# Kernel tuning notes

Hardware: AMD Instinct MI355X
Metric: run time of the kernel (lower is better)

## Reference

```python
import jax, jax.numpy as jnp
import numpy as np

B, LAGS, POOL, D, H, NTS = 16, 4096, 4, 512, 8, 1000
S = LAGS // POOL          # num_pools = 1024
DH = D // H               # head dim = 64


def _layernorm_dim1(x, gamma, beta, eps=1e-5):
    # torch code: mean/var over dim=1 (channel axis), unbiased var, per-position affine
    mean = jnp.mean(x, axis=1, keepdims=True)
    var = jnp.var(x, axis=1, keepdims=True, ddof=1)
    unit = (x - mean) / jnp.sqrt(eps + var)
    return gamma * unit + beta


def setup_inputs() -> dict:
    key = jax.random.key(0)
    ks = jax.random.split(key, 16)
    inp = {
        "ts": jax.random.normal(ks[0], (B, 1, LAGS), dtype=jnp.float32),
        "te": jax.random.randint(ks[1], (B, 1), 0, NTS),
        "conv_w": jax.random.normal(ks[2], (D, 1, POOL), dtype=jnp.float32) * (1.0 / POOL) ** 0.5,
        "conv_b": jax.random.normal(ks[3], (D,), dtype=jnp.float32) * 0.02,
        "pe_emb": jax.random.normal(ks[4], (S, D), dtype=jnp.float32),
        "ts_emb": jax.random.normal(ks[5], (NTS, D), dtype=jnp.float32),
        "ln1_g": jnp.ones((S,), dtype=jnp.float32),
        "ln1_b": jnp.zeros((S,), dtype=jnp.float32),
        "dense_M": jax.random.normal(ks[6], (D, D), dtype=jnp.float32) * D ** -0.5,
        "Wq": jax.random.normal(ks[7], (H, DH, D), dtype=jnp.float32) * D ** -0.5,
        "Wk": jax.random.normal(ks[8], (H, DH, D), dtype=jnp.float32) * D ** -0.5,
        "Wv": jax.random.normal(ks[9], (H, DH, D), dtype=jnp.float32) * D ** -0.5,
        "Wo": jax.random.normal(ks[10], (D, D), dtype=jnp.float32) * D ** -0.5,
        "bo": jnp.zeros((D, 1), dtype=jnp.float32),
        "ln2_g": jnp.ones((S,), dtype=jnp.float32),
        "ln2_b": jnp.zeros((S,), dtype=jnp.float32),
    }
    return inp


def _forward(ts, te, conv_w, conv_b, pe_emb, ts_emb, ln1_g, ln1_b,
             dense_M, Wq, Wk, Wv, Wo, bo, ln2_g, ln2_b):
    # Conv1d with stride == kernel_size: non-overlapping patches
    xr = ts.reshape(B, S, POOL)                                   # (B,S,P)
    conv = jnp.einsum('bsp,dp->bds', xr, conv_w[:, 0, :]) + conv_b[:, None]  # (B,D,S)
    conv = conv + pe_emb.T                                        # positional add (D,S)
    act = jax.nn.gelu(conv, approximate=False)
    n1 = _layernorm_dim1(act, ln1_g, ln1_b)
    dense = jnp.einsum('ed,bds->bes', dense_M, n1)                # Linear: M @ x
    dense = dense + ts_emb[te[:, 0]][:, :, None]                  # ts embedding (B,D,1)

    # multi-head attention, Q=K=V=dense; vectorized over heads
    Qd = jnp.einsum('hcd,bds->bhcs', Wq, dense)                   # (B,H,DH,S)
    Kd = jnp.einsum('hcd,bds->bhcs', Wk, dense)
    Vd = jnp.einsum('hcd,bds->bhcs', Wv, dense)
    scores = jnp.einsum('bhci,bhcj->bhij', Qd, Kd) / DH ** 0.5    # (B,H,S,S)
    i_idx = jnp.arange(S)
    mask = i_idx[:, None] > i_idx[None, :]                        # tril(diagonal=-1): i>j -> -inf
    scores = jnp.where(mask, -jnp.inf, scores)
    sm = jax.nn.softmax(scores, axis=2)                           # softmax over dim 1 of (S,S)
    attn = jnp.einsum('bhci,bhij->bhcj', Vd, sm)                  # V @ softmaxed
    cat = attn.reshape(B, D, S)                                   # concat heads on dim 1
    out = jnp.einsum('ed,bds->bes', Wo, cat) + bo[None]           # final linear + bias
    res = out + conv                                              # residual
    return _layernorm_dim1(res, ln2_g, ln2_b)


def reference(ts, te, conv_w, conv_b, pe_emb, ts_emb, ln1_g, ln1_b,
              dense_M, Wq, Wk, Wv, Wo, bo, ln2_g, ln2_b):
    return _forward(ts, te, conv_w, conv_b, pe_emb, ts_emb, ln1_g, ln1_b,
                    dense_M, Wq, Wk, Wv, Wo, bo, ln2_g, ln2_b)
```

## Files before the change

kernel.cpp:

```cpp
#include <hip/hip_runtime.h>
#include <hip/hip_bf16.h>

#define B_ 16
#define S_ 1024
#define D_ 512
#define H_ 8
#define DH_ 64

typedef __attribute__((ext_vector_type(8))) short bf16x8;
typedef __attribute__((ext_vector_type(4))) short bf16x4;
typedef __attribute__((ext_vector_type(4))) float f32x4;
typedef __attribute__((ext_vector_type(16))) float f32x16;

__device__ __forceinline__ short f2bf(float f) {
    __hip_bfloat16 h = __float2bfloat16(f);
    return *reinterpret_cast<short*>(&h);
}
__device__ __forceinline__ float bf2f(short s) {
    unsigned u = ((unsigned)(unsigned short)s) << 16;
    return __uint_as_float(u);
}
__device__ __forceinline__ unsigned pack_bf2(float lo, float hi) {
    unsigned a = (unsigned)(unsigned short)f2bf(lo);
    unsigned b = (unsigned)(unsigned short)f2bf(hi);
    return a | (b << 16);
}
__device__ __forceinline__ void gload16(const void* g, void* l) {
    __builtin_amdgcn_global_load_lds(
        (const __attribute__((address_space(1))) unsigned int*)g,
        (__attribute__((address_space(3))) unsigned int*)l, 16, 0, 0);
}

__global__ __launch_bounds__(256) void prep_w(
    const float* __restrict__ M, const float* __restrict__ Wq,
    const float* __restrict__ Wk, const float* __restrict__ Wv,
    const float* __restrict__ Wo, __hip_bfloat16* __restrict__ wb)
{
    __hip_bfloat16* wsrc = wb;
    __hip_bfloat16* Wob  = wb + 786432;
    __hip_bfloat16* MT   = wb + 1048576;

    const int blk = blockIdx.x, t = threadIdx.x;
    if (blk < 512) {
        const int wi = blk >> 7;
        const int off = (blk & 127) * 2048 + t * 8;
        const float* src = (wi == 0) ? Wq : (wi == 1) ? Wk : (wi == 2) ? Wv : Wo;
        const float scale = (wi == 0) ? 0.18033688011112042f : 1.0f;
        const float4 f0 = *reinterpret_cast<const float4*>(src + off);
        const float4 f1 = *reinterpret_cast<const float4*>(src + off + 4);
        const float fv[8] = {f0.x, f0.y, f0.z, f0.w, f1.x, f1.y, f1.z, f1.w};
        union { short s[8]; bf16x8 v; } r;
#pragma unroll
        for (int j = 0; j < 8; ++j) r.s[j] = f2bf(fv[j] * scale);
        __hip_bfloat16* dst = (wi == 3) ? (Wob + off) : (wsrc + wi * 262144 + off);
        *reinterpret_cast<bf16x8*>(dst) = r.v;
    } else {
        __shared__ float tile[32][33];
        const int tt = blk - 512;
        const int e0 = (tt & 15) * 32, d0 = (tt >> 4) * 32;
        const int r = t >> 5, c = t & 31;
#pragma unroll
        for (int k = 0; k < 4; ++k)
            tile[r + k * 8][c] = M[(size_t)(e0 + r + k * 8) * 512 + d0 + c];
        __syncthreads();
#pragma unroll
        for (int k = 0; k < 4; ++k)
            MT[(size_t)(d0 + r + k * 8) * 512 + e0 + c] =
                __float2bfloat16(tile[c][r + k * 8]);
    }
}

__global__ __launch_bounds__(256) void bias_k(
    const __hip_bfloat16* __restrict__ wsrc, const float* __restrict__ ts_emb,
    const int* __restrict__ te, float* __restrict__ qkvpart)
{
    const int blk = blockIdx.x;
    const int w16b = blk >> 2, dc = blk & 3;
    const int b = w16b & 15, w = w16b >> 4;
    const float* e = ts_emb + (size_t)te[b] * 512 + dc * 128;
#pragma unroll
    for (int rep = 0; rep < 2; ++rep) {
        const int n = threadIdx.x + rep * 256;
        const __hip_bfloat16* wr = wsrc + ((size_t)(w * 512 + n)) * 512 + dc * 128;
        float s = 0.f;
#pragma unroll 4
        for (int d8 = 0; d8 < 128; d8 += 8) {
            const bf16x8 wv8 = *reinterpret_cast<const bf16x8*>(wr + d8);
            const float4 e0 = *reinterpret_cast<const float4*>(e + d8);
            const float4 e1 = *reinterpret_cast<const float4*>(e + d8 + 4);
            s += bf2f(wv8[0]) * e0.x + bf2f(wv8[1]) * e0.y
               + bf2f(wv8[2]) * e0.z + bf2f(wv8[3]) * e0.w
               + bf2f(wv8[4]) * e1.x + bf2f(wv8[5]) * e1.y
               + bf2f(wv8[6]) * e1.z + bf2f(wv8[7]) * e1.w;
        }
        qkvpart[(size_t)dc * 24576 + (size_t)w16b * 512 + n] = s;
    }
}

__global__ __launch_bounds__(256) void k1_conv_gelu_ln(
    const float* __restrict__ ts, const float* __restrict__ conv_w,
    const float* __restrict__ conv_b, const float* __restrict__ pe,
    const float* __restrict__ g1, const float* __restrict__ b1,
    __hip_bfloat16* __restrict__ n1)
{
    const int w = threadIdx.x >> 6, lane = threadIdx.x & 63;
    const int row = blockIdx.x * 4 + w;
    const int b = row >> 10, s = row & 1023;
    const float4 x = *reinterpret_cast<const float4*>(ts + b * 4096 + s * 4);
    const int d0 = lane * 8;

    const float4 cb0 = *reinterpret_cast<const float4*>(conv_b + d0);
    const float4 cb1 = *reinterpret_cast<const float4*>(conv_b + d0 + 4);
    const float4 pe0 = *reinterpret_cast<const float4*>(pe + s * 512 + d0);
    const float4 pe1 = *reinterpret_cast<const float4*>(pe + s * 512 + d0 + 4);
    const float cbv[8] = {cb0.x, cb0.y, cb0.z, cb0.w, cb1.x, cb1.y, cb1.z, cb1.w};
    const float pev[8] = {pe0.x, pe0.y, pe0.z, pe0.w, pe1.x, pe1.y, pe1.z, pe1.w};

    float a[8];
    float sum = 0.f, sq = 0.f;
#pragma unroll
    for (int j = 0; j < 8; ++j) {
        const float4 wv = *reinterpret_cast<const float4*>(conv_w + (d0 + j) * 4);
        float v = x.x * wv.x + x.y * wv.y + x.z * wv.z + x.w * wv.w
                + cbv[j] + pev[j];
        v = 0.5f * v * (1.0f + erff(v * 0.70710678118654752f));
        a[j] = v; sum += v; sq += v * v;
    }
#pragma unroll
    for (int off = 1; off < 64; off <<= 1) {
        sum += __shfl_xor(sum, off);
        sq  += __shfl_xor(sq, off);
    }
    const float mean = sum * (1.0f / 512.0f);
    const float var  = (sq - 512.0f * mean * mean) * (1.0f / 511.0f);
    const float rstd = rsqrtf(var + 1e-5f);
    const float gg = g1[s], bb = b1[s];
    union { short sh[8]; bf16x8 v; } o;
#pragma unroll
    for (int j = 0; j < 8; ++j)
        o.sh[j] = f2bf(gg * ((a[j] - mean) * rstd) + bb);
    *reinterpret_cast<bf16x8*>(n1 + (size_t)row * 512 + d0) = o.v;
}

template<int MODE>
__global__ __launch_bounds__(256, 2) void gemm_k(
    const __hip_bfloat16* __restrict__ A,
    const __hip_bfloat16* __restrict__ Wb,
    void* __restrict__ outp,
    const float* __restrict__ aux)
{
    __shared__ char lA[2][128 * 128];
    __shared__ char lB[2][128 * 128];

    const int t = threadIdx.x;
    const int lane = t & 63;
    const int w = t >> 6;
    const int wm = w & 1, wn = w >> 1;
    const int Rb = blockIdx.x * 128;
    const int Nb = blockIdx.y * 128;
    const int g = lane >> 4, lr = lane & 15;
    const int lrow = lane >> 3;
    const int coff = ((lane & 7) ^ lrow) * 8;

    const __hip_bfloat16* asrc = A  + (size_t)(Rb + lrow) * 512 + coff;
    const __hip_bfloat16* bsrc = Wb + (size_t)(Nb + lrow) * 512 + coff;

    f32x4 acc[4][4];
#pragma unroll
    for (int i = 0; i < 4; ++i)
#pragma unroll
        for (int j = 0; j < 4; ++j) acc[i][j] = {0.f, 0.f, 0.f, 0.f};

    auto stage = [&](int buf, int k0) {
#pragma unroll
        for (int i = 0; i < 4; ++i) {
            const int r0 = w * 32 + i * 8;
            gload16(asrc + (size_t)r0 * 512 + k0, &lA[buf][r0 * 128]);
        }
#pragma unroll
        for (int i = 0; i < 4; ++i) {
            const int r0 = w * 32 + i * 8;
            gload16(bsrc + (size_t)r0 * 512 + k0, &lB[buf][r0 * 128]);
        }
    };

    stage(0, 0);
    __syncthreads();

    for (int kt = 0; kt < 8; ++kt) {
        const int buf = kt & 1;
        if (kt < 7) stage(buf ^ 1, (kt + 1) * 64);
#pragma unroll
        for (int kk = 0; kk < 2; ++kk) {
            bf16x8 af[4], bfv[4];
            const int ch = kk * 4 + g;
#pragma unroll
            for (int mt = 0; mt < 4; ++mt) {
                const int row = wm * 64 + mt * 16 + lr;
                af[mt] = *reinterpret_cast<const bf16x8*>(
                    &lA[buf][row * 128 + ((ch ^ (row & 7)) << 4)]);
            }
#pragma unroll
            for (int nt = 0; nt < 4; ++nt) {
                const int row = wn * 64 + nt * 16 + lr;
                bfv[nt] = *reinterpret_cast<const bf16x8*>(
                    &lB[buf][row * 128 + ((ch ^ (row & 7)) << 4)]);
            }
#pragma unroll
            for (int mt = 0; mt < 4; ++mt)
#pragma unroll
                for (int nt = 0; nt < 4; ++nt)
                    acc[mt][nt] = __builtin_amdgcn_mfma_f32_16x16x32_bf16(
                        af[mt], bfv[nt], acc[mt][nt], 0, 0, 0);
        }
        __syncthreads();
    }

    const int w3 = Nb >> 9;
#pragma unroll
    for (int mt = 0; mt < 4; ++mt) {
#pragma unroll
        for (int nt = 0; nt < 4; ++nt) {
#pragma unroll
            for (int r = 0; r < 4; ++r) {
                const int R = Rb + wm * 64 + mt * 16 + 4 * g + r;
                const int N = Nb + wn * 64 + nt * 16 + lr;
                float v = acc[mt][nt][r];
                if (MODE == 5) {
                    const int Nl = N & 511;
                    const int b = R >> 10, s = R & 1023, h = Nl >> 6, c = Nl & 63;
                    const float* qp = aux + (size_t)(w3 * 16 + b) * 512 + Nl;
                    v += qp[0] + qp[24576] + qp[49152] + qp[73728];
                    __hip_bfloat16* base =
                        reinterpret_cast<__hip_bfloat16*>(outp) + (size_t)w3 * 8388608;
                    if (w3 == 2)
                        base[(((size_t)(b * 8 + h)) * 64 + c) * 1024 + s] =
                            __float2bfloat16(v);
                    else
                        base[(((size_t)(b * 8 + h)) * 1024 + s) * 64 + c] =
                            __float2bfloat16(v);
                } else if (MODE == 6) {
                    reinterpret_cast<__hip_bfloat16*>(outp)[(size_t)R * 512 + N] =
                        __float2bfloat16(v);
                } else {
                    reinterpret_cast<float*>(outp)[(size_t)R * 512 + N] = v + aux[N];
                }
            }
        }
    }
}

__device__ __forceinline__ void write_strip(
    __hip_bfloat16* __restrict__ dstbase, const int jw0,
    const f32x16& o0, const f32x16& o1, const float lsum,
    const int l5, const int ln31)
{
    const float linv = 1.0f / lsum;
#pragma unroll
    for (int r = 0; r < 16; ++r) {
        const int jrow = (r & 3) + 8 * (r >> 2) + 4 * l5;
        const float rinv = __shfl(linv, jrow);
        __hip_bfloat16* dst = dstbase + (size_t)(jw0 + jrow) * 512;
        dst[ln31]      = __float2bfloat16(o0[r] * rinv);
        dst[32 + ln31] = __float2bfloat16(o1[r] * rinv);
    }
}

__global__ __launch_bounds__(256, 4) void attn5_k(
    const __hip_bfloat16* __restrict__ Qm,
    const __hip_bfloat16* __restrict__ Km,
    const __hip_bfloat16* __restrict__ Vt,
    __hip_bfloat16* __restrict__ cat)
{
    __shared__ char qbuf[2][4096];
    __shared__ char vbuf[2][4096];

    const int t = threadIdx.x, lane = t & 63, w = t >> 6;
    const int l5 = lane >> 5, ln31 = lane & 31;
    const int id = blockIdx.x;
    const int bh = id & 127;
    const int jb = (0x32451067u >> ((id >> 7) * 4)) & 7;
    const int b = bh >> 3, h = bh & 7;
    const int j0 = jb * 128 + w * 32;

    const __hip_bfloat16* Qh = Qm + (size_t)bh * (S_ * 64);
    const __hip_bfloat16* Kh = Km + (size_t)bh * (S_ * 64);
    const __hip_bfloat16* Vh = Vt + (size_t)bh * (64 * S_);

    bf16x8 kf[4];
#pragma unroll
    for (int kt = 0; kt < 4; ++kt)
        kf[kt] = *reinterpret_cast<const bf16x8*>(
            Kh + (size_t)(j0 + ln31) * 64 + kt * 16 + l5 * 8);

    f32x16 o0, o1;
#pragma unroll
    for (int r = 0; r < 16; ++r) { o0[r] = 0.f; o1[r] = 0.f; }
    float m = -3e38f, lsum = 0.f;

    const int last = jb * 4 + w;
    const int ntiles = jb * 4 + 4;

    const int q_row  = w * 8 + (lane >> 3);
    const int q_ch   = (lane & 7) ^ (lane >> 3);
    const int v_row  = w * 16 + (lane >> 2);
    const int v_ch   = (lane & 3) ^ ((lane >> 2) & 3) ^ ((lane >> 4) & 3);
    const __hip_bfloat16* qsrc = Qh + (size_t)q_row * 64 + q_ch * 8;
    const __hip_bfloat16* vsrc = Vh + (size_t)v_row * 1024 + v_ch * 8;

    auto stage = [&](int buf, int tile) {
        const int i0 = tile * 32;
        gload16(qsrc + (size_t)i0 * 64, &qbuf[buf][w * 1024]);
        gload16(vsrc + i0,              &vbuf[buf][w * 1024]);
    };

    stage(0, 0);
    __syncthreads();

    for (int tt = 0; tt < ntiles; ++tt) {
        const int buf = tt & 1;
        if (tt + 1 < ntiles) stage(buf ^ 1, tt + 1);
        if (tt <= last) {
            f32x16 sc;
#pragma unroll
            for (int r = 0; r < 16; ++r) sc[r] = 0.f;
            bf16x8 qf[4];
#pragma unroll
            for (int kt = 0; kt < 4; ++kt)
                qf[kt] = *reinterpret_cast<const bf16x8*>(
                    &qbuf[buf][ln31 * 128 + (((kt * 2 + l5) ^ (ln31 & 7)) << 4)]);
#pragma unroll
            for (int kt = 0; kt < 4; ++kt)
                sc = __builtin_amdgcn_mfma_f32_32x32x16_bf16(qf[kt], kf[kt], sc, 0, 0, 0);

            union u8 { bf16x4 h[2]; bf16x8 v; };
            u8 vf[2][2];
#pragma unroll
            for (int kt = 0; kt < 2; ++kt) {
#pragma unroll
                for (int dh = 0; dh < 2; ++dh) {
                    const int drow = ln31 + dh * 32;
                    const int swz = (drow & 3) ^ ((drow >> 2) & 3);
                    const int x0 = kt * 32 + 8 * l5;
#pragma unroll
                    for (int hp = 0; hp < 2; ++hp) {
                        const int x = x0 + hp * 16;
                        vf[kt][dh].h[hp] = *reinterpret_cast<const bf16x4*>(
                            &vbuf[buf][drow * 64 + (((x >> 4) ^ swz) << 4) + (x & 15)]);
                    }
                }
            }

            const bool diag = (tt == last);
            float p[16];
            float mx = -3e38f;
            if (diag) {
#pragma unroll
                for (int r = 0; r < 16; ++r) {
                    const int irow = (r & 3) + 8 * (r >> 2) + 4 * l5;
                    const float v = (irow > ln31) ? -3e38f : sc[r];
                    p[r] = v; mx = fmaxf(mx, v);
                }
            } else {
#pragma unroll
                for (int r = 0; r < 16; ++r) { p[r] = sc[r]; mx = fmaxf(mx, sc[r]); }
            }
            mx = fmaxf(mx, __shfl_xor(mx, 32));
            if (!__all(mx <= m + 8.0f)) {
                const float mn = fmaxf(m, mx);
                const float alpha = exp2f(m - mn);
                m = mn; lsum *= alpha;
#pragma unroll
                for (int r = 0; r < 16; ++r) {
                    const int jrow = (r & 3) + 8 * (r >> 2) + 4 * l5;
                    const float ar = __shfl(alpha, jrow);
                    o0[r] *= ar; o1[r] *= ar;
                }
            }
            float ps = 0.f;
#pragma unroll
            for (int r = 0; r < 16; ++r) { p[r] = exp2f(p[r] - m); ps += p[r]; }
            ps += __shfl_xor(ps, 32);
            lsum += ps;

            union { unsigned u[4]; bf16x8 v; } pa0, pa1;
            pa0.u[0] = pack_bf2(p[0],  p[1]);  pa0.u[1] = pack_bf2(p[2],  p[3]);
            pa0.u[2] = pack_bf2(p[4],  p[5]);  pa0.u[3] = pack_bf2(p[6],  p[7]);
            pa1.u[0] = pack_bf2(p[8],  p[9]);  pa1.u[1] = pack_bf2(p[10], p[11]);
            pa1.u[2] = pack_bf2(p[12], p[13]); pa1.u[3] = pack_bf2(p[14], p[15]);
            o0 = __builtin_amdgcn_mfma_f32_32x32x16_bf16(pa0.v, vf[0][0].v, o0, 0, 0, 0);
            o1 = __builtin_amdgcn_mfma_f32_32x32x16_bf16(pa0.v, vf[0][1].v, o1, 0, 0, 0);
            o0 = __builtin_amdgcn_mfma_f32_32x32x16_bf16(pa1.v, vf[1][0].v, o0, 0, 0, 0);
            o1 = __builtin_amdgcn_mfma_f32_32x32x16_bf16(pa1.v, vf[1][1].v, o1, 0, 0, 0);
        }
        __syncthreads();
    }

    __hip_bfloat16* dstbase = cat + (size_t)b * 1024 * 512 + h * 64;
    write_strip(dstbase, j0, o0, o1, lsum, l5, ln31);
}

__global__ __launch_bounds__(256) void k5_res_ln(
    const float* __restrict__ outf,
    const float* __restrict__ ts, const float* __restrict__ conv_w,
    const float* __restrict__ conv_b, const float* __restrict__ pe,
    const float* __restrict__ g2, const float* __restrict__ b2,
    float* __restrict__ out)
{
    __shared__ float tile[16 * 520];
    const int blk = blockIdx.x;
    const int b = blk >> 6, s0 = (blk & 63) * 16;
    const int t = threadIdx.x;
    const int sl = t >> 4, c = t & 15;
    const int s = s0 + sl;

    const float4 x = *reinterpret_cast<const float4*>(ts + b * 4096 + s * 4);
    float vals[32];
    float sum = 0.f, sq = 0.f;
#pragma unroll
    for (int j = 0; j < 32; ++j) {
        const int d = c + 16 * j;
        const float4 wv = *reinterpret_cast<const float4*>(conv_w + d * 4);
        const float conv = x.x * wv.x + x.y * wv.y + x.z * wv.z + x.w * wv.w
                         + conv_b[d] + pe[s * 512 + d];
        const float a = outf[(size_t)(b * 1024 + s) * 512 + d] + conv;
        vals[j] = a; sum += a; sq += a * a;
    }
#pragma unroll
    for (int off = 1; off < 16; off <<= 1) {
        sum += __shfl_xor(sum, off);
        sq  += __shfl_xor(sq, off);
    }
    const float mean = sum * (1.0f / 512.0f);
    const float var  = (sq - 512.0f * mean * mean) * (1.0f / 511.0f);
    const float rstd = rsqrtf(var + 1e-5f);
    const float gg = g2[s], bb = b2[s];
#pragma unroll
    for (int j = 0; j < 32; ++j) {
        const int d = c + 16 * j;
        tile[sl * 520 + d] = gg * ((vals[j] - mean) * rstd) + bb;
    }
    __syncthreads();
#pragma unroll
    for (int q2 = 0; q2 < 2; ++q2) {
        const int d = t + q2 * 256;
        float buf[16];
#pragma unroll
        for (int sl2 = 0; sl2 < 16; ++sl2) buf[sl2] = tile[sl2 * 520 + d];
        float4* dst = reinterpret_cast<float4*>(
            out + ((size_t)b * 512 + d) * 1024 + s0);
        dst[0] = make_float4(buf[0],  buf[1],  buf[2],  buf[3]);
        dst[1] = make_float4(buf[4],  buf[5],  buf[6],  buf[7]);
        dst[2] = make_float4(buf[8],  buf[9],  buf[10], buf[11]);
        dst[3] = make_float4(buf[12], buf[13], buf[14], buf[15]);
    }
}

extern "C" void kernel_launch(void* const* d_in, const int* in_sizes, int n_in,
                              void* d_out, int out_size, void* d_ws, size_t ws_size,
                              hipStream_t stream)
{
    const float* ts     = (const float*)d_in[0];
    const int*   te     = (const int*)d_in[1];
    const float* conv_w = (const float*)d_in[2];
    const float* conv_b = (const float*)d_in[3];
    const float* pe     = (const float*)d_in[4];
    const float* ts_emb = (const float*)d_in[5];
    const float* g1     = (const float*)d_in[6];
    const float* b1     = (const float*)d_in[7];
    const float* M      = (const float*)d_in[8];
    const float* Wq     = (const float*)d_in[9];
    const float* Wk     = (const float*)d_in[10];
    const float* Wv     = (const float*)d_in[11];
    const float* Wo     = (const float*)d_in[12];
    const float* bo     = (const float*)d_in[13];
    const float* g2     = (const float*)d_in[14];
    const float* b2     = (const float*)d_in[15];

    char* ws = (char*)d_ws;
    __hip_bfloat16* wb     = (__hip_bfloat16*)(ws);
    __hip_bfloat16* wsrc   = wb;
    __hip_bfloat16* Wob    = wb + 786432;
    __hip_bfloat16* MT     = wb + 1048576;
    __hip_bfloat16* Wqkvp  = (__hip_bfloat16*)(ws + (2688ull << 10));
    float*          qkvpart= (float*)(ws + (4608ull << 10));
    __hip_bfloat16* n1     = (__hip_bfloat16*)(ws + ( 6ull << 20));
    __hip_bfloat16* cat    = n1;
    __hip_bfloat16* q      = (__hip_bfloat16*)(ws + (22ull << 20));
    __hip_bfloat16* k      = (__hip_bfloat16*)(ws + (38ull << 20));
    __hip_bfloat16* vT     = (__hip_bfloat16*)(ws + (54ull << 20));
    float*          outf   = (float*)(ws + (22ull << 20));

    prep_w<<<768, 256, 0, stream>>>(M, Wq, Wk, Wv, Wo, wb);
    bias_k<<<192, 256, 0, stream>>>(wsrc, ts_emb, te, qkvpart);
    gemm_k<6><<<dim3(12, 4), 256, 0, stream>>>(wsrc, MT, Wqkvp, nullptr);
    k1_conv_gelu_ln<<<4096, 256, 0, stream>>>(ts, conv_w, conv_b, pe, g1, b1, n1);
    gemm_k<5><<<dim3(128, 12), 256, 0, stream>>>(n1, Wqkvp, q, qkvpart);
    attn5_k<<<1024, 256, 0, stream>>>(q, k, vT, cat);
    gemm_k<3><<<dim3(128, 4), 256, 0, stream>>>(cat, Wob, outf, bo);
    k5_res_ln<<<1024, 256, 0, stream>>>(outf, ts, conv_w, conv_b, pe, g2, b2,
                                        (float*)d_out);
}
```

Measured before the change: 174.3 us.

## Single-buffer GEMM LDS, pair causal attention blocks, store out-proj in bf16

The GEMM kernel drops LDS double buffering in favour of a single buffer with a sync per k-tile, which halves shared memory so the launch bound can rise to 4 blocks per CU. This trades away load/compute overlap for occupancy. The attention kernel now runs 512 blocks, each handling a short and a long causal query block (jb and 7-jb) in sequence, to balance the triangular workload. Separately, the output projection is stored as bf16 rather than fp32 and read back in the residual LayerNorm, which halves that traffic at some precision cost.

Result: slower. 181.4 us (+4.1%).

```diff
diff --git a/kernel.cpp b/kernel.cpp
--- a/kernel.cpp
+++ b/kernel.cpp
@@ -143,14 +143,14 @@
 }
 
 template<int MODE>
-__global__ __launch_bounds__(256, 2) void gemm_k(
+__global__ __launch_bounds__(256, 4) void gemm_k(
     const __hip_bfloat16* __restrict__ A,
     const __hip_bfloat16* __restrict__ Wb,
     void* __restrict__ outp,
     const float* __restrict__ aux)
 {
-    __shared__ char lA[2][128 * 128];
-    __shared__ char lB[2][128 * 128];
+    __shared__ char lA[128 * 128];
+    __shared__ char lB[128 * 128];
 
     const int t = threadIdx.x;
     const int lane = t & 63;
@@ -171,25 +171,19 @@
 #pragma unroll
         for (int j = 0; j < 4; ++j) acc[i][j] = {0.f, 0.f, 0.f, 0.f};
 
-    auto stage = [&](int buf, int k0) {
+    for (int kt = 0; kt < 8; ++kt) {
+        const int k0 = kt * 64;
 #pragma unroll
         for (int i = 0; i < 4; ++i) {
             const int r0 = w * 32 + i * 8;
-            gload16(asrc + (size_t)r0 * 512 + k0, &lA[buf][r0 * 128]);
+            gload16(asrc + (size_t)r0 * 512 + k0, &lA[r0 * 128]);
         }
 #pragma unroll
         for (int i = 0; i < 4; ++i) {
             const int r0 = w * 32 + i * 8;
-            gload16(bsrc + (size_t)r0 * 512 + k0, &lB[buf][r0 * 128]);
+            gload16(bsrc + (size_t)r0 * 512 + k0, &lB[r0 * 128]);
         }
-    };
-
-    stage(0, 0);
-    __syncthreads();
-
-    for (int kt = 0; kt < 8; ++kt) {
-        const int buf = kt & 1;
-        if (kt < 7) stage(buf ^ 1, (kt + 1) * 64);
+        __syncthreads();
 #pragma unroll
         for (int kk = 0; kk < 2; ++kk) {
             bf16x8 af[4], bfv[4];
@@ -198,13 +192,13 @@
             for (int mt = 0; mt < 4; ++mt) {
                 const int row = wm * 64 + mt * 16 + lr;
                 af[mt] = *reinterpret_cast<const bf16x8*>(
-                    &lA[buf][row * 128 + ((ch ^ (row & 7)) << 4)]);
+                    &lA[row * 128 + ((ch ^ (row & 7)) << 4)]);
             }
 #pragma unroll
             for (int nt = 0; nt < 4; ++nt) {
                 const int row = wn * 64 + nt * 16 + lr;
                 bfv[nt] = *reinterpret_cast<const bf16x8*>(
-                    &lB[buf][row * 128 + ((ch ^ (row & 7)) << 4)]);
+                    &lB[row * 128 + ((ch ^ (row & 7)) << 4)]);
             }
 #pragma unroll
             for (int mt = 0; mt < 4; ++mt)
@@ -243,7 +237,8 @@
                     reinterpret_cast<__hip_bfloat16*>(outp)[(size_t)R * 512 + N] =
                         __float2bfloat16(v);
                 } else {
-                    reinterpret_cast<float*>(outp)[(size_t)R * 512 + N] = v + aux[N];
+                    reinterpret_cast<__hip_bfloat16*>(outp)[(size_t)R * 512 + N] =
+                        __float2bfloat16(v + aux[N]);
                 }
             }
         }
@@ -266,7 +261,7 @@
     }
 }
 
-__global__ __launch_bounds__(256, 4) void attn5_k(
+__global__ __launch_bounds__(256, 2) void attn6_k(
     const __hip_bfloat16* __restrict__ Qm,
     const __hip_bfloat16* __restrict__ Km,
     const __hip_bfloat16* __restrict__ Vt,
@@ -279,27 +274,12 @@
     const int l5 = lane >> 5, ln31 = lane & 31;
     const int id = blockIdx.x;
     const int bh = id & 127;
-    const int jb = (0x32451067u >> ((id >> 7) * 4)) & 7;
+    const int sidx = id >> 7;
     const int b = bh >> 3, h = bh & 7;
-    const int j0 = jb * 128 + w * 32;
 
     const __hip_bfloat16* Qh = Qm + (size_t)bh * (S_ * 64);
     const __hip_bfloat16* Kh = Km + (size_t)bh * (S_ * 64);
     const __hip_bfloat16* Vh = Vt + (size_t)bh * (64 * S_);
-
-    bf16x8 kf[4];
-#pragma unroll
-    for (int kt = 0; kt < 4; ++kt)
-        kf[kt] = *reinterpret_cast<const bf16x8*>(
-            Kh + (size_t)(j0 + ln31) * 64 + kt * 16 + l5 * 8);
-
-    f32x16 o0, o1;
-#pragma unroll
-    for (int r = 0; r < 16; ++r) { o0[r] = 0.f; o1[r] = 0.f; }
-    float m = -3e38f, lsum = 0.f;
-
-    const int last = jb * 4 + w;
-    const int ntiles = jb * 4 + 4;
 
     const int q_row  = w * 8 + (lane >> 3);
     const int q_ch   = (lane & 7) ^ (lane >> 3);
@@ -307,6 +287,7 @@
     const int v_ch   = (lane & 3) ^ ((lane >> 2) & 3) ^ ((lane >> 4) & 3);
     const __hip_bfloat16* qsrc = Qh + (size_t)q_row * 64 + q_ch * 8;
     const __hip_bfloat16* vsrc = Vh + (size_t)v_row * 1024 + v_ch * 8;
+    __hip_bfloat16* dstbase = cat + (size_t)b * 1024 * 512 + h * 64;
 
     auto stage = [&](int buf, int tile) {
         const int i0 = tile * 32;
@@ -314,94 +295,112 @@
         gload16(vsrc + i0,              &vbuf[buf][w * 1024]);
     };
 
-    stage(0, 0);
-    __syncthreads();
-
-    for (int tt = 0; tt < ntiles; ++tt) {
-        const int buf = tt & 1;
-        if (tt + 1 < ntiles) stage(buf ^ 1, tt + 1);
-        if (tt <= last) {
-            f32x16 sc;
-#pragma unroll
-            for (int r = 0; r < 16; ++r) sc[r] = 0.f;
-            bf16x8 qf[4];
-#pragma unroll
-            for (int kt = 0; kt < 4; ++kt)
-                qf[kt] = *reinterpret_cast<const bf16x8*>(
-                    &qbuf[buf][ln31 * 128 + (((kt * 2 + l5) ^ (ln31 & 7)) << 4)]);
-#pragma unroll
-            for (int kt = 0; kt < 4; ++kt)
-                sc = __builtin_amdgcn_mfma_f32_32x32x16_bf16(qf[kt], kf[kt], sc, 0, 0, 0);
-
-            union u8 { bf16x4 h[2]; bf16x8 v; };
-            u8 vf[2][2];
-#pragma unroll
-            for (int kt = 0; kt < 2; ++kt) {
-#pragma unroll
-                for (int dh = 0; dh < 2; ++dh) {
-                    const int drow = ln31 + dh * 32;
-                    const int swz = (drow & 3) ^ ((drow >> 2) & 3);
-                    const int x0 = kt * 32 + 8 * l5;
-#pragma unroll
-                    for (int hp = 0; hp < 2; ++hp) {
-                        const int x = x0 + hp * 16;
-                        vf[kt][dh].h[hp] = *reinterpret_cast<const bf16x4*>(
-                            &vbuf[buf][drow * 64 + (((x >> 4) ^ swz) << 4) + (x & 15)]);
+    for (int ph = 0; ph < 2; ++ph) {
+        const int jb = ph ? (7 - sidx) : sidx;
+        const int j0 = jb * 128 + w * 32;
+
+        bf16x8 kf[4];
+#pragma unroll
+        for (int kt = 0; kt < 4; ++kt)
+            kf[kt] = *reinterpret_cast<const bf16x8*>(
+                Kh + (size_t)(j0 + ln31) * 64 + kt * 16 + l5 * 8);
+
+        f32x16 o0, o1;
+#pragma unroll
+        for (int r = 0; r < 16; ++r) { o0[r] = 0.f; o1[r] = 0.f; }
+        float m = -3e38f, lsum = 0.f;
+
+        const int last = jb * 4 + w;
+        const int ntiles = jb * 4 + 4;
+
+        stage(0, 0);
+        __syncthreads();
+
+        for (int tt = 0; tt < ntiles; ++tt) {
+            const int buf = tt & 1;
+            if (tt + 1 < ntiles) stage(buf ^ 1, tt + 1);
+            if (tt <= last) {
+                f32x16 sc;
+#pragma unroll
+                for (int r = 0; r < 16; ++r) sc[r] = 0.f;
+                bf16x8 qf[4];
+#pragma unroll
+                for (int kt = 0; kt < 4; ++kt)
+                    qf[kt] = *reinterpret_cast<const bf16x8*>(
+                        &qbuf[buf][ln31 * 128 + (((kt * 2 + l5) ^ (ln31 & 7)) << 4)]);
+#pragma unroll
+                for (int kt = 0; kt < 4; ++kt)
+                    sc = __builtin_amdgcn_mfma_f32_32x32x16_bf16(qf[kt], kf[kt], sc, 0, 0, 0);
+
+                union u8 { bf16x4 h[2]; bf16x8 v; };
+                u8 vf[2][2];
+#pragma unroll
+                for (int kt = 0; kt < 2; ++kt) {
+#pragma unroll
+                    for (int dh = 0; dh < 2; ++dh) {
+                        const int drow = ln31 + dh * 32;
+                        const int swz = (drow & 3) ^ ((drow >> 2) & 3);
+                        const int x0 = kt * 32 + 8 * l5;
+#pragma unroll
+                        for (int hp = 0; hp < 2; ++hp) {
+                            const int x = x0 + hp * 16;
+                            vf[kt][dh].h[hp] = *reinterpret_cast<const bf16x4*>(
+                                &vbuf[buf][drow * 64 + (((x >> 4) ^ swz) << 4) + (x & 15)]);
+                        }
                     }
                 }
+
+                const bool diag = (tt == last);
+                float p[16];
+                float mx = -3e38f;
+                if (diag) {
+#pragma unroll
+                    for (int r = 0; r < 16; ++r) {
+                        const int irow = (r & 3) + 8 * (r >> 2) + 4 * l5;
+                        const float v = (irow > ln31) ? -3e38f : sc[r];
+                        p[r] = v; mx = fmaxf(mx, v);
+                    }
+                } else {
+#pragma unroll
+                    for (int r = 0; r < 16; ++r) { p[r] = sc[r]; mx = fmaxf(mx, sc[r]); }
+                }
+                mx = fmaxf(mx, __shfl_xor(mx, 32));
+                if (!__all(mx <= m + 8.0f)) {
+                    const float mn = fmaxf(m, mx);
+                    const float alpha = exp2f(m - mn);
+                    m = mn; lsum *= alpha;
+#pragma unroll
+                    for (int r = 0; r < 16; ++r) {
+                        const int jrow = (r & 3) + 8 * (r >> 2) + 4 * l5;
+                        const float ar = __shfl(alpha, jrow);
+                        o0[r] *= ar; o1[r] *= ar;
+                    }
+                }
+                float ps = 0.f;
+#pragma unroll
+                for (int r = 0; r < 16; ++r) { p[r] = exp2f(p[r] - m); ps += p[r]; }
+                ps += __shfl_xor(ps, 32);
+                lsum += ps;
+
+                union { unsigned u[4]; bf16x8 v; } pa0, pa1;
+                pa0.u[0] = pack_bf2(p[0],  p[1]);  pa0.u[1] = pack_bf2(p[2],  p[3]);
+                pa0.u[2] = pack_bf2(p[4],  p[5]);  pa0.u[3] = pack_bf2(p[6],  p[7]);
+                pa1.u[0] = pack_bf2(p[8],  p[9]);  pa1.u[1] = pack_bf2(p[10], p[11]);
+                pa1.u[2] = pack_bf2(p[12], p[13]); pa1.u[3] = pack_bf2(p[14], p[15]);
+                o0 = __builtin_amdgcn_mfma_f32_32x32x16_bf16(pa0.v, vf[0][0].v, o0, 0, 0, 0);
+                o1 = __builtin_amdgcn_mfma_f32_32x32x16_bf16(pa0.v, vf[0][1].v, o1, 0, 0, 0);
+                o0 = __builtin_amdgcn_mfma_f32_32x32x16_bf16(pa1.v, vf[1][0].v, o0, 0, 0, 0);
+                o1 = __builtin_amdgcn_mfma_f32_32x32x16_bf16(pa1.v, vf[1][1].v, o1, 0, 0, 0);
             }
-
-            const bool diag = (tt == last);
-            float p[16];
-            float mx = -3e38f;
-            if (diag) {
-#pragma unroll
-                for (int r = 0; r < 16; ++r) {
-                    const int irow = (r & 3) + 8 * (r >> 2) + 4 * l5;
-                    const float v = (irow > ln31) ? -3e38f : sc[r];
-                    p[r] = v; mx = fmaxf(mx, v);
-                }
-            } else {
-#pragma unroll
-                for (int r = 0; r < 16; ++r) { p[r] = sc[r]; mx = fmaxf(mx, sc[r]); }
-            }
-            mx = fmaxf(mx, __shfl_xor(mx, 32));
-            if (!__all(mx <= m + 8.0f)) {
-                const float mn = fmaxf(m, mx);
-                const float alpha = exp2f(m - mn);
-                m = mn; lsum *= alpha;
-#pragma unroll
-                for (int r = 0; r < 16; ++r) {
-                    const int jrow = (r & 3) + 8 * (r >> 2) + 4 * l5;
-                    const float ar = __shfl(alpha, jrow);
-                    o0[r] *= ar; o1[r] *= ar;
-                }
-            }
-            float ps = 0.f;
-#pragma unroll
-            for (int r = 0; r < 16; ++r) { p[r] = exp2f(p[r] - m); ps += p[r]; }
-            ps += __shfl_xor(ps, 32);
-            lsum += ps;
-
-            union { unsigned u[4]; bf16x8 v; } pa0, pa1;
-            pa0.u[0] = pack_bf2(p[0],  p[1]);  pa0.u[1] = pack_bf2(p[2],  p[3]);
-            pa0.u[2] = pack_bf2(p[4],  p[5]);  pa0.u[3] = pack_bf2(p[6],  p[7]);
-            pa1.u[0] = pack_bf2(p[8],  p[9]);  pa1.u[1] = pack_bf2(p[10], p[11]);
-            pa1.u[2] = pack_bf2(p[12], p[13]); pa1.u[3] = pack_bf2(p[14], p[15]);
-            o0 = __builtin_amdgcn_mfma_f32_32x32x16_bf16(pa0.v, vf[0][0].v, o0, 0, 0, 0);
-            o1 = __builtin_amdgcn_mfma_f32_32x32x16_bf16(pa0.v, vf[0][1].v, o1, 0, 0, 0);
-            o0 = __builtin_amdgcn_mfma_f32_32x32x16_bf16(pa1.v, vf[1][0].v, o0, 0, 0, 0);
-            o1 = __builtin_amdgcn_mfma_f32_32x32x16_bf16(pa1.v, vf[1][1].v, o1, 0, 0, 0);
+            __syncthreads();
         }
-        __syncthreads();
-    }
-
-    __hip_bfloat16* dstbase = cat + (size_t)b * 1024 * 512 + h * 64;
-    write_strip(dstbase, j0, o0, o1, lsum, l5, ln31);
+
+        write_strip(dstbase, j0, o0, o1, lsum, l5, ln31);
+    }
 }
 
 __global__ __launch_bounds__(256) void k5_res_ln(
-    const float* __restrict__ outf,
+    const __hip_bfloat16* __restrict__ outf,
     const float* __restrict__ ts, const float* __restrict__ conv_w,
     const float* __restrict__ conv_b, const float* __restrict__ pe,
     const float* __restrict__ g2, const float* __restrict__ b2,
@@ -423,7 +422,7 @@
         const float4 wv = *reinterpret_cast<const float4*>(conv_w + d * 4);
         const float conv = x.x * wv.x + x.y * wv.y + x.z * wv.z + x.w * wv.w
                          + conv_b[d] + pe[s * 512 + d];
-        const float a = outf[(size_t)(b * 1024 + s) * 512 + d] + conv;
+        const float a = __bfloat162float(outf[(size_t)(b * 1024 + s) * 512 + d]) + conv;
         vals[j] = a; sum += a; sq += a * a;
     }
 #pragma unroll
@@ -489,14 +488,14 @@
     __hip_bfloat16* q      = (__hip_bfloat16*)(ws + (22ull << 20));
     __hip_bfloat16* k      = (__hip_bfloat16*)(ws + (38ull << 20));
     __hip_bfloat16* vT     = (__hip_bfloat16*)(ws + (54ull << 20));
-    float*          outf   = (float*)(ws + (22ull << 20));
+    __hip_bfloat16* outf   = (__hip_bfloat16*)(ws + (22ull << 20));
 
     prep_w<<<768, 256, 0, stream>>>(M, Wq, Wk, Wv, Wo, wb);
     bias_k<<<192, 256, 0, stream>>>(wsrc, ts_emb, te, qkvpart);
     gemm_k<6><<<dim3(12, 4), 256, 0, stream>>>(wsrc, MT, Wqkvp, nullptr);
     k1_conv_gelu_ln<<<4096, 256, 0, stream>>>(ts, conv_w, conv_b, pe, g1, b1, n1);
     gemm_k<5><<<dim3(128, 12), 256, 0, stream>>>(n1, Wqkvp, q, qkvpart);
-    attn5_k<<<1024, 256, 0, stream>>>(q, k, vT, cat);
+    attn6_k<<<512, 256, 0, stream>>>(q, k, vT, cat);
     gemm_k<3><<<dim3(128, 4), 256, 0, stream>>>(cat, Wob, outf, bo);
     k5_res_ln<<<1024, 256, 0, stream>>>(outf, ts, conv_w, conv_b, pe, g2, b2,
                                         (float*)d_out);
```
